# Performance work log

Hardware: AMD Instinct MI355X
Metric: run time of the kernel (lower is better)

Reference implementation:

```python
import jax, jax.numpy as jnp
import numpy as np

N = 100000
E = 1600000
F_IN = 512
H1, C1 = 8, 8          # conv1: 8 heads x 8 channels, concat -> 64
H2, C2 = 1, 16         # conv2: 1 head x num_classes=16, mean
NEG_SLOPE = 0.2


def setup_inputs() -> dict:
    key = jax.random.key(0)
    ks = jax.random.split(key, 10)
    x = jax.random.normal(ks[0], (N, F_IN), dtype=jnp.float32)
    edge_index = jax.random.randint(ks[1], (2, E), 0, N, dtype=jnp.int64)
    s1 = 1.0 / np.sqrt(F_IN)
    s2 = 1.0 / np.sqrt(H1 * C1)
    W1 = jax.random.normal(ks[2], (F_IN, H1 * C1), dtype=jnp.float32) * s1
    a1_src = jax.random.normal(ks[3], (H1, C1), dtype=jnp.float32) * 0.1
    a1_dst = jax.random.normal(ks[4], (H1, C1), dtype=jnp.float32) * 0.1
    b1 = jnp.zeros((H1 * C1,), dtype=jnp.float32)
    W2 = jax.random.normal(ks[5], (H1 * C1, H2 * C2), dtype=jnp.float32) * s2
    a2_src = jax.random.normal(ks[6], (H2, C2), dtype=jnp.float32) * 0.1
    a2_dst = jax.random.normal(ks[7], (H2, C2), dtype=jnp.float32) * 0.1
    b2 = jnp.zeros((C2,), dtype=jnp.float32)
    return {"x": x, "edge_index": edge_index, "W1": W1, "a1_src": a1_src,
            "a1_dst": a1_dst, "b1": b1, "W2": W2, "a2_src": a2_src,
            "a2_dst": a2_dst, "b2": b2}


def _add_self_loops(edge_index, n):
    loops = jnp.arange(n, dtype=edge_index.dtype)
    return jnp.concatenate([edge_index, jnp.stack([loops, loops])], axis=1)


def gat_conv(x, edge_index, W, a_src, a_dst, bias, concat):
    # x: [N, Fin]; W: [Fin, H*C]; a_*: [H, C]
    n = x.shape[0]
    H, C = a_src.shape
    h = (x @ W).reshape(n, H, C)                      # [N, H, C]
    al_src = jnp.einsum('nhc,hc->nh', h, a_src)       # [N, H]
    al_dst = jnp.einsum('nhc,hc->nh', h, a_dst)
    src, dst = edge_index[0], edge_index[1]
    e = al_src[src] + al_dst[dst]                     # [E, H]
    e = jnp.where(e > 0, e, NEG_SLOPE * e)            # LeakyReLU
    # segment softmax over destination nodes
    m = jax.ops.segment_max(e, dst, num_segments=n)   # [N, H]
    ex = jnp.exp(e - m[dst])
    s = jax.ops.segment_sum(ex, dst, num_segments=n)  # [N, H]
    alpha = ex / s[dst]                               # [E, H]
    msg = h[src] * alpha[:, :, None]                  # [E, H, C]
    out = jax.ops.segment_sum(msg, dst, num_segments=n)  # [N, H, C]
    if concat:
        out = out.reshape(n, H * C)
    else:
        out = out.mean(axis=1)
    return out + bias


def reference(x, edge_index, W1, a1_src, a1_dst, b1, W2, a2_src, a2_dst, b2):
    ei = _add_self_loops(edge_index, x.shape[0])
    h = gat_conv(x, ei, W1, a1_src, a1_dst, b1, concat=True)
    h = jax.nn.elu(h)
    h = gat_conv(h, ei, W2, a2_src, a2_dst, b2, concat=False)
    return jax.nn.log_softmax(h, axis=1)
```

## Files before the change

kernel.cpp:

```cpp
#include <hip/hip_runtime.h>
#include <hip/hip_fp16.h>
#include <math.h>

#define F_IN 512
#define NHEAD1 8
#define NC1 8
#define F1 64
#define NC2 16
#define NEG_SLOPE 0.2f
#define BSHIFT 7
#define PART_G 512
#define BUILD_CAP 4608

typedef _Float16 v8h __attribute__((ext_vector_type(8)));
typedef float v4f __attribute__((ext_vector_type(4)));

static __device__ __forceinline__ float leaky(float v) {
    return v > 0.0f ? v : NEG_SLOPE * v;
}

__global__ __launch_bounds__(256) void k_prep(const float* __restrict__ W,
                                              _Float16* __restrict__ w1t) {
    int idx = blockIdx.x * 256 + threadIdx.x;
    if (idx < 64 * 512) {
        int c = idx >> 9, k = idx & 511;
        w1t[idx] = (_Float16)W[k * 64 + c];
    }
}

__global__ __launch_bounds__(256) void k_gemm1(const float* __restrict__ x,
                                               const _Float16* __restrict__ w1t,
                                               const float* __restrict__ a1s,
                                               const float* __restrict__ a1d,
                                               float* __restrict__ h1,
                                               float* __restrict__ al1s,
                                               float* __restrict__ al1d, int N) {
    __shared__ _Float16 xs[64][72];
    __shared__ _Float16 ws[64][72];
    const int tid = threadIdx.x;
    const int lane = tid & 63;
    const int wv = tid >> 6;
    const int row0 = blockIdx.x * 64;
    const int srow = tid >> 2;
    const int skq = (tid & 3) * 16;
    v4f acc[4] = {};

    for (int k0 = 0; k0 < F_IN; k0 += 64) {
        int gr = row0 + srow;
        float4 v0, v1, v2, v3;
        if (gr < N) {
            const float* p = x + (size_t)gr * F_IN + k0 + skq;
            v0 = *(const float4*)p;       v1 = *(const float4*)(p + 4);
            v2 = *(const float4*)(p + 8); v3 = *(const float4*)(p + 12);
        } else {
            v0 = make_float4(0.f, 0.f, 0.f, 0.f); v1 = v0; v2 = v0; v3 = v0;
        }
        const _Float16* q = w1t + (size_t)srow * F_IN + k0 + skq;
        v8h wa = *(const v8h*)q;
        v8h wb = *(const v8h*)(q + 8);
        v8h xa, xb;
        xa[0] = (_Float16)v0.x; xa[1] = (_Float16)v0.y;
        xa[2] = (_Float16)v0.z; xa[3] = (_Float16)v0.w;
        xa[4] = (_Float16)v1.x; xa[5] = (_Float16)v1.y;
        xa[6] = (_Float16)v1.z; xa[7] = (_Float16)v1.w;
        xb[0] = (_Float16)v2.x; xb[1] = (_Float16)v2.y;
        xb[2] = (_Float16)v2.z; xb[3] = (_Float16)v2.w;
        xb[4] = (_Float16)v3.x; xb[5] = (_Float16)v3.y;
        xb[6] = (_Float16)v3.z; xb[7] = (_Float16)v3.w;
        __syncthreads();
        *(v8h*)&xs[srow][skq]     = xa;
        *(v8h*)&xs[srow][skq + 8] = xb;
        *(v8h*)&ws[srow][skq]     = wa;
        *(v8h*)&ws[srow][skq + 8] = wb;
        __syncthreads();
        #pragma unroll
        for (int kk = 0; kk < 64; kk += 32) {
            v8h a = *(const v8h*)&xs[wv * 16 + (lane & 15)][kk + (lane >> 4) * 8];
            #pragma unroll
            for (int c4 = 0; c4 < 4; ++c4) {
                v8h b = *(const v8h*)&ws[c4 * 16 + (lane & 15)][kk + (lane >> 4) * 8];
                acc[c4] = __builtin_amdgcn_mfma_f32_16x16x32_f16(a, b, acc[c4], 0, 0, 0);
            }
        }
    }
    const int g = lane >> 4;
    const int cl = lane & 15;
    #pragma unroll
    for (int c4 = 0; c4 < 4; ++c4) {
        float asv = a1s[c4 * 16 + cl];
        float adv = a1d[c4 * 16 + cl];
        #pragma unroll
        for (int r = 0; r < 4; ++r) {
            int gr = row0 + wv * 16 + g * 4 + r;
            float vacc = acc[c4][r];
            float ps = vacc * asv, pd = vacc * adv;
            ps += __shfl_xor(ps, 1); ps += __shfl_xor(ps, 2); ps += __shfl_xor(ps, 4);
            pd += __shfl_xor(pd, 1); pd += __shfl_xor(pd, 2); pd += __shfl_xor(pd, 4);
            if (gr < N) {
                h1[(size_t)gr * F1 + c4 * 16 + cl] = vacc;
                if ((lane & 7) == 0) {
                    int head = c4 * 2 + (cl >> 3);
                    al1s[gr * 8 + head] = ps;
                    al1d[gr * 8 + head] = pd;
                }
            }
        }
    }
}

__global__ __launch_bounds__(256) void k_bcount(const int* __restrict__ ei,
                                                int* __restrict__ counts,
                                                int E, int NBUCK, int chunk) {
    __shared__ int cnt[1024];
    const int g = blockIdx.x, tid = threadIdx.x;
    for (int i = tid; i < NBUCK; i += 256) cnt[i] = 0;
    __syncthreads();
    int lo = g * chunk, hi = lo + chunk;
    if (hi > E) hi = E;
    for (int e = lo + tid; e < hi; e += 256)
        atomicAdd(&cnt[ei[E + e] >> BSHIFT], 1);
    __syncthreads();
    for (int k = tid; k < NBUCK; k += 256)
        counts[k * PART_G + g] = cnt[k];
}

__global__ __launch_bounds__(256) void k_scan_block(const int* __restrict__ in,
                                                    int* __restrict__ out,
                                                    int* __restrict__ blocksum, int L) {
    __shared__ int sdata[256];
    int t = threadIdx.x;
    int i = blockIdx.x * 256 + t;
    int v = (i < L) ? in[i] : 0;
    sdata[t] = v;
    __syncthreads();
    for (int off = 1; off < 256; off <<= 1) {
        int add = (t >= off) ? sdata[t - off] : 0;
        __syncthreads();
        sdata[t] += add;
        __syncthreads();
    }
    if (i < L) out[i] = sdata[t] - v;
    if (t == 255) blocksum[blockIdx.x] = sdata[t];
}

__global__ void k_scan_carry(const int* __restrict__ blocksum,
                             int* __restrict__ blockoffset, int NB) {
    int lane = threadIdx.x;
    int carry = 0;
    for (int base = 0; base < NB; base += 64) {
        int i = base + lane;
        int v = (i < NB) ? blocksum[i] : 0;
        int x = v;
        #pragma unroll
        for (int off = 1; off < 64; off <<= 1) {
            int y = __shfl_up(x, off);
            if (lane >= off) x += y;
        }
        if (i < NB) blockoffset[i] = carry + x - v;
        carry += __shfl(x, 63);
    }
}

__global__ __launch_bounds__(256) void k_bscatter(const int* __restrict__ ei,
                                                  const int* __restrict__ offs,
                                                  const int* __restrict__ boff,
                                                  unsigned* __restrict__ packed,
                                                  int E, int NBUCK, int chunk) {
    __shared__ int cur[1024];
    const int g = blockIdx.x, tid = threadIdx.x;
    for (int k = tid; k < NBUCK; k += 256) {
        int idx = k * PART_G + g;
        cur[k] = offs[idx] + boff[idx >> 8];
    }
    __syncthreads();
    int lo = g * chunk, hi = lo + chunk;
    if (hi > E) hi = E;
    for (int e = lo + tid; e < hi; e += 256) {
        int src = ei[e], dst = ei[E + e];
        int pos = atomicAdd(&cur[dst >> BSHIFT], 1);
        packed[pos] = ((unsigned)(dst & 127) << 20) | (unsigned)src;
    }
}

__global__ __launch_bounds__(256) void k_bbuild(const unsigned* __restrict__ packed,
                                                const int* __restrict__ offs,
                                                const int* __restrict__ boff,
                                                int* __restrict__ rowptr,
                                                int* __restrict__ esrc,
                                                int E, int N, int NBUCK) {
    __shared__ int sdeg[128], sinc[128], scur[128];
    __shared__ int sbuf[BUILD_CAP];
    const int k = blockIdx.x, tid = threadIdx.x;
    const int i0 = k * PART_G;
    const int s = offs[i0] + boff[i0 >> 8];
    int e;
    if (k + 1 < NBUCK) {
        int i1 = (k + 1) * PART_G;
        e = offs[i1] + boff[i1 >> 8];
    } else e = E;
    const int cnt = e - s;
    if (tid < 128) sdeg[tid] = 0;
    __syncthreads();
    for (int i = tid; i < cnt; i += 256)
        atomicAdd(&sdeg[packed[s + i] >> 20], 1);
    __syncthreads();
    if (tid < 128) sinc[tid] = sdeg[tid];
    __syncthreads();
    for (int off = 1; off < 128; off <<= 1) {
        int add = (tid < 128 && tid >= off) ? sinc[tid - off] : 0;
        __syncthreads();
        if (tid < 128) sinc[tid] += add;
        __syncthreads();
    }
    int nd = N - (k << BSHIFT);
    if (nd > 128) nd = 128;
    if (tid < nd) {
        int excl = sinc[tid] - sdeg[tid];
        rowptr[(k << BSHIFT) + tid] = s + excl;
        scur[tid] = excl;
    }
    if (k == 0 && tid == 0) rowptr[N] = E;
    __syncthreads();
    if (cnt <= BUILD_CAP) {
        for (int i = tid; i < cnt; i += 256) {
            unsigned p = packed[s + i];
            int pos = atomicAdd(&scur[p >> 20], 1);
            sbuf[pos] = (int)(p & 0xFFFFFu);
        }
        __syncthreads();
        for (int i = tid; i < cnt; i += 256) esrc[s + i] = sbuf[i];
    } else {
        for (int i = tid; i < cnt; i += 256) {
            unsigned p = packed[s + i];
            int pos = atomicAdd(&scur[p >> 20], 1);
            esrc[s + pos] = (int)(p & 0xFFFFFu);
        }
    }
}

__global__ __launch_bounds__(256) void k_agg1(
    const float* __restrict__ h1, const float* __restrict__ al1s,
    const float* __restrict__ al1d, const int* __restrict__ rowptr,
    const int* __restrict__ esrc, const float* __restrict__ b1,
    const float* __restrict__ W2, const float* __restrict__ a2s,
    const float* __restrict__ a2d, __half* __restrict__ h2h,
    float* __restrict__ al2s, float* __restrict__ al2d, int N) {
    const int lane = threadIdx.x & 63;
    const int wv = threadIdx.x >> 6;
    const int n = blockIdx.x * 4 + wv;
    if (n >= N) return;
    const int sub = lane >> 4;
    const int t = lane & 15;
    const int h = t >> 1;

    float4 w2r[4];
    #pragma unroll
    for (int j = 0; j < 4; ++j)
        w2r[j] = *(const float4*)(W2 + (4 * t + j) * NC2 + 4 * sub);
    const float4 b1v  = *(const float4*)(b1 + 4 * t);
    const float4 a2sv = *(const float4*)(a2s + 4 * sub);
    const float4 a2dv = *(const float4*)(a2d + 4 * sub);

    const float aldh = al1d[n * 8 + h];
    float s = 0.f, acc0 = 0.f, acc1 = 0.f, acc2 = 0.f, acc3 = 0.f;
    if (sub == 0) {
        float w0 = __expf(leaky(al1s[n * 8 + h] + aldh));
        float4 u = *(const float4*)(h1 + (size_t)n * F1 + t * 4);
        s = w0;
        acc0 = w0 * u.x; acc1 = w0 * u.y; acc2 = w0 * u.z; acc3 = w0 * u.w;
    }
    const int start = rowptr[n], end = rowptr[n + 1];
    for (int base = start; base < end; base += 64) {
        int cnt = end - base;
        if (cnt > 64) cnt = 64;
        int msrc = (lane < cnt) ? esrc[base + lane] : 0;
        for (int j4 = 0; j4 < cnt; j4 += 4) {
            int idx = j4 + sub;
            int src = __shfl(msrc, idx);
            float w = (idx < cnt) ? __expf(leaky(al1s[src * 8 + h] + aldh)) : 0.f;
            float4 u = *(const float4*)(h1 + (size_t)src * F1 + t * 4);
            s += w;
            acc0 = fmaf(w, u.x, acc0);
            acc1 = fmaf(w, u.y, acc1);
            acc2 = fmaf(w, u.z, acc2);
            acc3 = fmaf(w, u.w, acc3);
        }
    }
    #pragma unroll
    for (int off = 16; off < 64; off <<= 1) {
        s    += __shfl_xor(s, off);
        acc0 += __shfl_xor(acc0, off);
        acc1 += __shfl_xor(acc1, off);
        acc2 += __shfl_xor(acc2, off);
        acc3 += __shfl_xor(acc3, off);
    }
    float rs = 1.0f / s;
    float v0 = acc0 * rs + b1v.x; v0 = v0 > 0.f ? v0 : expm1f(v0);
    float v1 = acc1 * rs + b1v.y; v1 = v1 > 0.f ? v1 : expm1f(v1);
    float v2 = acc2 * rs + b1v.z; v2 = v2 > 0.f ? v2 : expm1f(v2);
    float v3 = acc3 * rs + b1v.w; v3 = v3 > 0.f ? v3 : expm1f(v3);
    float p0 = v0 * w2r[0].x + v1 * w2r[1].x + v2 * w2r[2].x + v3 * w2r[3].x;
    float p1 = v0 * w2r[0].y + v1 * w2r[1].y + v2 * w2r[2].y + v3 * w2r[3].y;
    float p2 = v0 * w2r[0].z + v1 * w2r[1].z + v2 * w2r[2].z + v3 * w2r[3].z;
    float p3 = v0 * w2r[0].w + v1 * w2r[1].w + v2 * w2r[2].w + v3 * w2r[3].w;
    #pragma unroll
    for (int off = 1; off < 16; off <<= 1) {
        p0 += __shfl_xor(p0, off);
        p1 += __shfl_xor(p1, off);
        p2 += __shfl_xor(p2, off);
        p3 += __shfl_xor(p3, off);
    }
    float ts = p0 * a2sv.x + p1 * a2sv.y + p2 * a2sv.z + p3 * a2sv.w;
    float td = p0 * a2dv.x + p1 * a2dv.y + p2 * a2dv.z + p3 * a2dv.w;
    ts += __shfl_xor(ts, 16); ts += __shfl_xor(ts, 32);
    td += __shfl_xor(td, 16); td += __shfl_xor(td, 32);
    if (t == 0) {
        union { __half2 h2v[2]; float2 f; } cv;
        cv.h2v[0] = __floats2half2_rn(p0, p1);
        cv.h2v[1] = __floats2half2_rn(p2, p3);
        *(float2*)(h2h + (size_t)n * NC2 + sub * 4) = cv.f;
    }
    if (lane == 0) { al2s[n] = ts; al2d[n] = td; }
}

__global__ __launch_bounds__(256) void k_agg2(
    const __half* __restrict__ h2h, const float* __restrict__ al2s,
    const float* __restrict__ al2d, const int* __restrict__ rowptr,
    const int* __restrict__ esrc, const float* __restrict__ b2,
    float* __restrict__ out, int N) {
    const int lane = threadIdx.x & 63;
    const int wv = threadIdx.x >> 6;
    const int n = blockIdx.x * 4 + wv;
    if (n >= N) return;
    const int sub = lane >> 2;
    const int t = lane & 3;
    const float ald = al2d[n];
    float s = 0.f, a0 = 0.f, a1 = 0.f, a2 = 0.f, a3 = 0.f;
    if (sub == 0) {
        float w0 = __expf(leaky(al2s[n] + ald));
        float2 raw0 = *(const float2*)(h2h + (size_t)n * NC2 + 4 * t);
        const __half2* hp = (const __half2*)&raw0;
        float2 c01 = __half22float2(hp[0]);
        float2 c23 = __half22float2(hp[1]);
        s = w0;
        a0 = w0 * c01.x; a1 = w0 * c01.y;
        a2 = w0 * c23.x; a3 = w0 * c23.y;
    }
    const int start = rowptr[n], end = rowptr[n + 1];
    for (int base = start; base < end; base += 64) {
        int cnt = end - base;
        if (cnt > 64) cnt = 64;
        int msrc = (lane < cnt) ? esrc[base + lane] : 0;
        for (int j16 = 0; j16 < cnt; j16 += 16) {
            int idx = j16 + sub;
            int src = __shfl(msrc, idx);
            float w = (idx < cnt) ? __expf(leaky(al2s[src] + ald)) : 0.f;
            float2 raw = *(const float2*)(h2h + (size_t)src * NC2 + 4 * t);
            const __half2* hp = (const __half2*)&raw;
            float2 c01 = __half22float2(hp[0]);
            float2 c23 = __half22float2(hp[1]);
            s += w;
            a0 = fmaf(w, c01.x, a0);
            a1 = fmaf(w, c01.y, a1);
            a2 = fmaf(w, c23.x, a2);
            a3 = fmaf(w, c23.y, a3);
        }
    }
    #pragma unroll
    for (int off = 4; off < 64; off <<= 1) {
        s  += __shfl_xor(s, off);
        a0 += __shfl_xor(a0, off);
        a1 += __shfl_xor(a1, off);
        a2 += __shfl_xor(a2, off);
        a3 += __shfl_xor(a3, off);
    }
    float rs = 1.0f / s;
    const float4 b2v = *(const float4*)(b2 + 4 * t);
    float v0 = a0 * rs + b2v.x;
    float v1 = a1 * rs + b2v.y;
    float v2 = a2 * rs + b2v.z;
    float v3 = a3 * rs + b2v.w;
    float mm = fmaxf(fmaxf(v0, v1), fmaxf(v2, v3));
    #pragma unroll
    for (int off = 1; off < 4; off <<= 1) mm = fmaxf(mm, __shfl_xor(mm, off));
    float se = __expf(v0 - mm) + __expf(v1 - mm) + __expf(v2 - mm) + __expf(v3 - mm);
    #pragma unroll
    for (int off = 1; off < 4; off <<= 1) se += __shfl_xor(se, off);
    float l = logf(se) + mm;
    if (sub == 0)
        *(float4*)(out + (size_t)n * NC2 + 4 * t) =
            make_float4(v0 - l, v1 - l, v2 - l, v3 - l);
}

extern "C" void kernel_launch(void* const* d_in, const int* in_sizes, int n_in,
                              void* d_out, int out_size, void* d_ws, size_t ws_size,
                              hipStream_t stream) {
    const float* x      = (const float*)d_in[0];
    const int*   ei     = (const int*)d_in[1];
    const float* W1     = (const float*)d_in[2];
    const float* a1_src = (const float*)d_in[3];
    const float* a1_dst = (const float*)d_in[4];
    const float* b1     = (const float*)d_in[5];
    const float* W2     = (const float*)d_in[6];
    const float* a2_src = (const float*)d_in[7];
    const float* a2_dst = (const float*)d_in[8];
    const float* b2     = (const float*)d_in[9];
    float* out = (float*)d_out;

    const int N = in_sizes[0] / F_IN;
    const int E = in_sizes[1] / 2;
    const int NH = N * NHEAD1;
    const int NBUCK = (N + 127) >> BSHIFT;
    const int L = NBUCK * PART_G;
    const int NB = (L + 255) / 256;
    const int chunk = (E + PART_G - 1) / PART_G;

    char* base = (char*)d_ws;
    size_t off = 0;
    auto alloc = [&](size_t bytes, size_t align) -> void* {
        off = (off + align - 1) & ~(align - 1);
        void* p = base + off; off += bytes; return p;
    };
    float* h1   = (float*)alloc((size_t)N * F1 * 4, 16);
    float* al1s = (float*)alloc((size_t)NH * 4, 16);
    float* al1d = (float*)alloc((size_t)NH * 4, 16);
    __half* h2h = (__half*)alloc((size_t)N * NC2 * 2, 16);
    float* al2s = (float*)alloc((size_t)N * 4, 16);
    float* al2d = (float*)alloc((size_t)N * 4, 16);
    int* rowptr = (int*)alloc((size_t)(N + 1) * 4, 16);
    int* esrc   = (int*)alloc((size_t)E * 4, 16);
    _Float16* w1t = (_Float16*)alloc((size_t)64 * F_IN * 2, 16);
    char* tbase = (char*)h1;
    unsigned* packed = (unsigned*)tbase;
    int* counts   = (int*)(tbase + (size_t)E * 4);
    int* offs     = counts + L;
    int* blocksum = offs + L;
    int* boffset  = blocksum + NB;

    auto blocks = [](long long cnt, int b) { return (int)((cnt + b - 1) / b); };

    k_bcount<<<PART_G, 256, 0, stream>>>(ei, counts, E, NBUCK, chunk);
    k_scan_block<<<NB, 256, 0, stream>>>(counts, offs, blocksum, L);
    k_scan_carry<<<1, 64, 0, stream>>>(blocksum, boffset, NB);
    k_bscatter<<<PART_G, 256, 0, stream>>>(ei, offs, boffset, packed, E, NBUCK, chunk);
    k_bbuild<<<NBUCK, 256, 0, stream>>>(packed, offs, boffset, rowptr, esrc, E, N, NBUCK);

    k_prep<<<128, 256, 0, stream>>>(W1, w1t);
    k_gemm1<<<dim3((N + 63) / 64), dim3(256), 0, stream>>>(x, w1t, a1_src, a1_dst,
                                                           h1, al1s, al1d, N);
    k_agg1<<<blocks(N, 4), 256, 0, stream>>>(h1, al1s, al1d, rowptr, esrc,
                                             b1, W2, a2_src, a2_dst,
                                             h2h, al2s, al2d, N);
    k_agg2<<<blocks(N, 4), 256, 0, stream>>>(h2h, al2s, al2d, rowptr, esrc, b2, out, N);
}
```

Before: 544.7 us.

## Replace bucketed two-pass CSR build with global-atomic degree count and scatter

```diff
diff --git a/kernel.cpp b/kernel.cpp
--- a/kernel.cpp
+++ b/kernel.cpp
@@ -8,9 +8,6 @@
 #define F1 64
 #define NC2 16
 #define NEG_SLOPE 0.2f
-#define BSHIFT 7
-#define PART_G 512
-#define BUILD_CAP 4608
 
 typedef _Float16 v8h __attribute__((ext_vector_type(8)));
 typedef float v4f __attribute__((ext_vector_type(4)));
@@ -108,20 +105,12 @@
     }
 }
 
-__global__ __launch_bounds__(256) void k_bcount(const int* __restrict__ ei,
-                                                int* __restrict__ counts,
-                                                int E, int NBUCK, int chunk) {
-    __shared__ int cnt[1024];
-    const int g = blockIdx.x, tid = threadIdx.x;
-    for (int i = tid; i < NBUCK; i += 256) cnt[i] = 0;
-    __syncthreads();
-    int lo = g * chunk, hi = lo + chunk;
-    if (hi > E) hi = E;
-    for (int e = lo + tid; e < hi; e += 256)
-        atomicAdd(&cnt[ei[E + e] >> BSHIFT], 1);
-    __syncthreads();
-    for (int k = tid; k < NBUCK; k += 256)
-        counts[k * PART_G + g] = cnt[k];
+__global__ __launch_bounds__(256) void k_deg(const int* __restrict__ ei,
+                                             int* __restrict__ deg, int E) {
+    int i = blockIdx.x * 256 + threadIdx.x;
+    int stride = gridDim.x * 256;
+    for (int e = i; e < E; e += stride)
+        atomicAdd(&deg[ei[E + e]], 1);
 }
 
 __global__ __launch_bounds__(256) void k_scan_block(const int* __restrict__ in,
@@ -161,80 +150,28 @@
     }
 }
 
-__global__ __launch_bounds__(256) void k_bscatter(const int* __restrict__ ei,
-                                                  const int* __restrict__ offs,
-                                                  const int* __restrict__ boff,
-                                                  unsigned* __restrict__ packed,
-                                                  int E, int NBUCK, int chunk) {
-    __shared__ int cur[1024];
-    const int g = blockIdx.x, tid = threadIdx.x;
-    for (int k = tid; k < NBUCK; k += 256) {
-        int idx = k * PART_G + g;
-        cur[k] = offs[idx] + boff[idx >> 8];
-    }
-    __syncthreads();
-    int lo = g * chunk, hi = lo + chunk;
-    if (hi > E) hi = E;
-    for (int e = lo + tid; e < hi; e += 256) {
+__global__ __launch_bounds__(256) void k_addback(int* __restrict__ rowptr,
+                                                 int* __restrict__ cursor,
+                                                 const int* __restrict__ boff,
+                                                 int N, int E) {
+    int i = blockIdx.x * 256 + threadIdx.x;
+    if (i < N) {
+        int v = rowptr[i] + boff[i >> 8];
+        rowptr[i] = v;
+        cursor[i] = v;
+    }
+    if (i == 0) rowptr[N] = E;
+}
+
+__global__ __launch_bounds__(256) void k_scatter(const int* __restrict__ ei,
+                                                 int* __restrict__ cursor,
+                                                 int* __restrict__ esrc, int E) {
+    int i = blockIdx.x * 256 + threadIdx.x;
+    int stride = gridDim.x * 256;
+    for (int e = i; e < E; e += stride) {
         int src = ei[e], dst = ei[E + e];
-        int pos = atomicAdd(&cur[dst >> BSHIFT], 1);
-        packed[pos] = ((unsigned)(dst & 127) << 20) | (unsigned)src;
-    }
-}
-
-__global__ __launch_bounds__(256) void k_bbuild(const unsigned* __restrict__ packed,
-                                                const int* __restrict__ offs,
-                                                const int* __restrict__ boff,
-                                                int* __restrict__ rowptr,
-                                                int* __restrict__ esrc,
-                                                int E, int N, int NBUCK) {
-    __shared__ int sdeg[128], sinc[128], scur[128];
-    __shared__ int sbuf[BUILD_CAP];
-    const int k = blockIdx.x, tid = threadIdx.x;
-    const int i0 = k * PART_G;
-    const int s = offs[i0] + boff[i0 >> 8];
-    int e;
-    if (k + 1 < NBUCK) {
-        int i1 = (k + 1) * PART_G;
-        e = offs[i1] + boff[i1 >> 8];
-    } else e = E;
-    const int cnt = e - s;
-    if (tid < 128) sdeg[tid] = 0;
-    __syncthreads();
-    for (int i = tid; i < cnt; i += 256)
-        atomicAdd(&sdeg[packed[s + i] >> 20], 1);
-    __syncthreads();
-    if (tid < 128) sinc[tid] = sdeg[tid];
-    __syncthreads();
-    for (int off = 1; off < 128; off <<= 1) {
-        int add = (tid < 128 && tid >= off) ? sinc[tid - off] : 0;
-        __syncthreads();
-        if (tid < 128) sinc[tid] += add;
-        __syncthreads();
-    }
-    int nd = N - (k << BSHIFT);
-    if (nd > 128) nd = 128;
-    if (tid < nd) {
-        int excl = sinc[tid] - sdeg[tid];
-        rowptr[(k << BSHIFT) + tid] = s + excl;
-        scur[tid] = excl;
-    }
-    if (k == 0 && tid == 0) rowptr[N] = E;
-    __syncthreads();
-    if (cnt <= BUILD_CAP) {
-        for (int i = tid; i < cnt; i += 256) {
-            unsigned p = packed[s + i];
-            int pos = atomicAdd(&scur[p >> 20], 1);
-            sbuf[pos] = (int)(p & 0xFFFFFu);
-        }
-        __syncthreads();
-        for (int i = tid; i < cnt; i += 256) esrc[s + i] = sbuf[i];
-    } else {
-        for (int i = tid; i < cnt; i += 256) {
-            unsigned p = packed[s + i];
-            int pos = atomicAdd(&scur[p >> 20], 1);
-            esrc[s + pos] = (int)(p & 0xFFFFFu);
-        }
+        int pos = atomicAdd(&cursor[dst], 1);
+        esrc[pos] = src;
     }
 }
 
@@ -295,10 +232,10 @@
         acc3 += __shfl_xor(acc3, off);
     }
     float rs = 1.0f / s;
-    float v0 = acc0 * rs + b1v.x; v0 = v0 > 0.f ? v0 : expm1f(v0);
-    float v1 = acc1 * rs + b1v.y; v1 = v1 > 0.f ? v1 : expm1f(v1);
-    float v2 = acc2 * rs + b1v.z; v2 = v2 > 0.f ? v2 : expm1f(v2);
-    float v3 = acc3 * rs + b1v.w; v3 = v3 > 0.f ? v3 : expm1f(v3);
+    float v0 = acc0 * rs + b1v.x; v0 = v0 > 0.f ? v0 : __expf(v0) - 1.0f;
+    float v1 = acc1 * rs + b1v.y; v1 = v1 > 0.f ? v1 : __expf(v1) - 1.0f;
+    float v2 = acc2 * rs + b1v.z; v2 = v2 > 0.f ? v2 : __expf(v2) - 1.0f;
+    float v3 = acc3 * rs + b1v.w; v3 = v3 > 0.f ? v3 : __expf(v3) - 1.0f;
     float p0 = v0 * w2r[0].x + v1 * w2r[1].x + v2 * w2r[2].x + v3 * w2r[3].x;
     float p1 = v0 * w2r[0].y + v1 * w2r[1].y + v2 * w2r[2].y + v3 * w2r[3].y;
     float p2 = v0 * w2r[0].z + v1 * w2r[1].z + v2 * w2r[2].z + v3 * w2r[3].z;
@@ -386,7 +323,7 @@
     float se = __expf(v0 - mm) + __expf(v1 - mm) + __expf(v2 - mm) + __expf(v3 - mm);
     #pragma unroll
     for (int off = 1; off < 4; off <<= 1) se += __shfl_xor(se, off);
-    float l = logf(se) + mm;
+    float l = __logf(se) + mm;
     if (sub == 0)
         *(float4*)(out + (size_t)n * NC2 + 4 * t) =
             make_float4(v0 - l, v1 - l, v2 - l, v3 - l);
@@ -410,10 +347,7 @@
     const int N = in_sizes[0] / F_IN;
     const int E = in_sizes[1] / 2;
     const int NH = N * NHEAD1;
-    const int NBUCK = (N + 127) >> BSHIFT;
-    const int L = NBUCK * PART_G;
-    const int NB = (L + 255) / 256;
-    const int chunk = (E + PART_G - 1) / PART_G;
+    const int NB2 = (N + 255) / 256;
 
     char* base = (char*)d_ws;
     size_t off = 0;
@@ -430,20 +364,18 @@
     int* rowptr = (int*)alloc((size_t)(N + 1) * 4, 16);
     int* esrc   = (int*)alloc((size_t)E * 4, 16);
     _Float16* w1t = (_Float16*)alloc((size_t)64 * F_IN * 2, 16);
-    char* tbase = (char*)h1;
-    unsigned* packed = (unsigned*)tbase;
-    int* counts   = (int*)(tbase + (size_t)E * 4);
-    int* offs     = counts + L;
-    int* blocksum = offs + L;
-    int* boffset  = blocksum + NB;
+    int* cursor   = (int*)h1;
+    int* blocksum = cursor + N;
+    int* boffset  = blocksum + NB2;
 
     auto blocks = [](long long cnt, int b) { return (int)((cnt + b - 1) / b); };
 
-    k_bcount<<<PART_G, 256, 0, stream>>>(ei, counts, E, NBUCK, chunk);
-    k_scan_block<<<NB, 256, 0, stream>>>(counts, offs, blocksum, L);
-    k_scan_carry<<<1, 64, 0, stream>>>(blocksum, boffset, NB);
-    k_bscatter<<<PART_G, 256, 0, stream>>>(ei, offs, boffset, packed, E, NBUCK, chunk);
-    k_bbuild<<<NBUCK, 256, 0, stream>>>(packed, offs, boffset, rowptr, esrc, E, N, NBUCK);
+    hipMemsetAsync(cursor, 0, (size_t)N * 4, stream);
+    k_deg<<<2048, 256, 0, stream>>>(ei, cursor, E);
+    k_scan_block<<<NB2, 256, 0, stream>>>(cursor, rowptr, blocksum, N);
+    k_scan_carry<<<1, 64, 0, stream>>>(blocksum, boffset, NB2);
+    k_addback<<<NB2, 256, 0, stream>>>(rowptr, cursor, boffset, N, E);
+    k_scatter<<<2048, 256, 0, stream>>>(ei, cursor, esrc, E);
 
     k_prep<<<128, 256, 0, stream>>>(W1, w1t);
     k_gemm1<<<dim3((N + 63) / 64), dim3(256), 0, stream>>>(x, w1t, a1_src, a1_dst,
```

After: 686.9 us. 26.1% more time.
